# Kernel optimization log

Hardware: AMD Instinct MI355X
Metric: run time of the kernel (lower is better)

## Reference

```python
import jax, jax.numpy as jnp
import numpy as np

D_MODEL = 2048
N_HEADS = 32
N_KV_GROUPS = 8
D_HEAD = D_MODEL // N_HEADS  # 64
HEADS_PER_GROUP = N_HEADS // N_KV_GROUPS  # 4
BATCH, SEQ = 2, 2048


def setup_inputs() -> dict:
    key = jax.random.key(0)
    ks = jax.random.split(key, 5)
    s = 0.02
    return {
        "x": jax.random.normal(ks[0], (BATCH, SEQ, D_MODEL), jnp.float32),
        "W_q": jax.random.normal(ks[1], (N_HEADS * D_HEAD, D_MODEL), jnp.float32) * s,
        "W_k": jax.random.normal(ks[2], (N_KV_GROUPS * D_HEAD, D_MODEL), jnp.float32) * s,
        "W_v": jax.random.normal(ks[3], (N_KV_GROUPS * D_HEAD, D_MODEL), jnp.float32) * s,
        "W_o": jax.random.normal(ks[4], (D_MODEL, D_MODEL), jnp.float32) * s,
    }


def reference(x, W_q, W_k, W_v, W_o):
    B, S, _ = x.shape
    # Projections (nn.Linear: y = x @ W.T)
    Q = (x @ W_q.T).reshape(B, S, N_HEADS, D_HEAD)          # (B,S,H,D)
    K = (x @ W_k.T).reshape(B, S, N_KV_GROUPS, D_HEAD)       # (B,S,G,D)
    V = (x @ W_v.T).reshape(B, S, N_KV_GROUPS, D_HEAD)
    # Group Q heads: (B, G, Hg, S, D) so each KV group serves Hg query heads
    Qg = Q.transpose(0, 2, 1, 3).reshape(B, N_KV_GROUPS, HEADS_PER_GROUP, S, D_HEAD)
    Kg = K.transpose(0, 2, 1, 3)  # (B,G,S,D)
    Vg = V.transpose(0, 2, 1, 3)
    scale = 1.0 / np.sqrt(D_HEAD).astype(np.float32)
    # scores: (B,G,Hg,S,S) == expanded-KV scores without replicating K/V
    scores = jnp.einsum('bghqd,bgkd->bghqk', Qg, Kg) * scale
    weights = jax.nn.softmax(scores, axis=-1)
    context = jnp.einsum('bghqk,bgkd->bghqd', weights, Vg)   # (B,G,Hg,S,D)
    # back to (B,S,d_model)
    context = context.reshape(B, N_HEADS, S, D_HEAD).transpose(0, 2, 1, 3).reshape(B, S, D_MODEL)
    return context @ W_o.T
```

## Files before the change

kernel.cpp:

```cpp
#include <hip/hip_runtime.h>
#include <hip/hip_bf16.h>
#include <stdint.h>
#include <stddef.h>

typedef __hip_bfloat16 bf16;
typedef short bf16x8 __attribute__((ext_vector_type(8)));
typedef float f32x4 __attribute__((ext_vector_type(4)));

#define BB 2
#define SS 2048
#define DM 2048
#define NH 32
#define NG 8
#define DH 64
#define ROWS (BB * SS)
#define NQK 2560

#define ALPHA_QK 0.4246609001440095f

__device__ __forceinline__ void gload_lds16(const void* g, void* l) {
  __builtin_amdgcn_global_load_lds((const __attribute__((address_space(1))) void*)g,
                                   (__attribute__((address_space(3))) void*)l, 16, 0, 0);
}

__device__ __forceinline__ unsigned cvt_pk_bf16(float lo, float hi) {
  unsigned r;
  asm("v_cvt_pk_bf16_f32 %0, %1, %2" : "=v"(r) : "v"(lo), "v"(hi));
  return r;
}

__global__ __launch_bounds__(256) void cvt_all(const float* __restrict__ x,
                                               const float* __restrict__ wq,
                                               const float* __restrict__ wk,
                                               const float* __restrict__ wv,
                                               const float* __restrict__ wo,
                                               bf16* __restrict__ xb,
                                               bf16* __restrict__ wqkb,
                                               bf16* __restrict__ wvb,
                                               bf16* __restrict__ wob) {
  const int i = blockIdx.x * 256 + threadIdx.x;
  const float* src;
  bf16* dst;
  if (i < 2097152)       { src = x  + (size_t)i * 4;              dst = xb   + (size_t)i * 4; }
  else if (i < 3145728)  { size_t j = i - 2097152; src = wq + j * 4; dst = wqkb + j * 4; }
  else if (i < 3407872)  { size_t j = i - 3145728; src = wk + j * 4; dst = wqkb + 4194304 + j * 4; }
  else if (i < 3670016)  { size_t j = i - 3407872; src = wv + j * 4; dst = wvb  + j * 4; }
  else                   { size_t j = i - 3670016; src = wo + j * 4; dst = wob  + j * 4; }
  float4 v = *reinterpret_cast<const float4*>(src);
  bf16 t0 = __float2bfloat16(v.x), t1 = __float2bfloat16(v.y);
  bf16 t2 = __float2bfloat16(v.z), t3 = __float2bfloat16(v.w);
  ushort4 o;
  o.x = *reinterpret_cast<unsigned short*>(&t0);
  o.y = *reinterpret_cast<unsigned short*>(&t1);
  o.z = *reinterpret_cast<unsigned short*>(&t2);
  o.w = *reinterpret_cast<unsigned short*>(&t3);
  *reinterpret_cast<ushort4*>(dst) = o;
}

__device__ __forceinline__ void store_elem(float* C, size_t i, float v) { C[i] = v; }
__device__ __forceinline__ void store_elem(bf16* C, size_t i, float v) { C[i] = __float2bfloat16(v); }

template <typename CT>
__global__ __launch_bounds__(256) void gemm_bt(const bf16* __restrict__ A,
                                               const bf16* __restrict__ Bm,
                                               CT* __restrict__ C,
                                               int M, int N, int K, float alpha) {
  const int t = threadIdx.x;
  const int w = t >> 6, lane = t & 63, lg = lane >> 4, lr = lane & 15;
  const int wr = w >> 1, wc = w & 1;
  const int nwg = gridDim.x * gridDim.y;
  const int flat = blockIdx.y * gridDim.x + blockIdx.x;
  const int swz = (flat & 7) * (nwg >> 3) + (flat >> 3);
  const int rowA = (swz / gridDim.x) * 128, rowB = (swz % gridDim.x) * 128;
  __shared__ __align__(16) bf16 sA[3][128 * 32];
  __shared__ __align__(16) bf16 sB[3][128 * 32];
  f32x4 acc[4][4] = {};

  auto STAGE = [&](int bi, int k0) {
#pragma unroll
    for (int i = 0; i < 2; ++i) {
      const int c = i * 256 + t;
      const int r = c >> 2, slot = c & 3;
      const int ck = slot ^ ((r >> 1) & 3);
      gload_lds16(A + (size_t)(rowA + r) * K + k0 + ck * 8, &sA[bi][c * 8]);
      gload_lds16(Bm + (size_t)(rowB + r) * K + k0 + ck * 8, &sB[bi][c * 8]);
    }
  };

  const int nt = K / 32;
  STAGE(0, 0);
  STAGE(1, 32);
  STAGE(2, 64);

  for (int i = 0; i < nt; ++i) {
    if (i <= nt - 3)      asm volatile("s_waitcnt vmcnt(8)" ::: "memory");
    else if (i == nt - 2) asm volatile("s_waitcnt vmcnt(4)" ::: "memory");
    else                  asm volatile("s_waitcnt vmcnt(0)" ::: "memory");
    __builtin_amdgcn_s_barrier();

    const int bi = i % 3;
    bf16x8 af[4], bfv[4];
#pragma unroll
    for (int mi = 0; mi < 4; ++mi) {
      const int r = wr * 64 + mi * 16 + lr;
      af[mi] = *(const bf16x8*)&sA[bi][r * 32 + (lg ^ ((r >> 1) & 3)) * 8];
    }
#pragma unroll
    for (int ni = 0; ni < 4; ++ni) {
      const int r = wc * 64 + ni * 16 + lr;
      bfv[ni] = *(const bf16x8*)&sB[bi][r * 32 + (lg ^ ((r >> 1) & 3)) * 8];
    }
    asm volatile("s_waitcnt lgkmcnt(0)" ::: "memory");
    __builtin_amdgcn_sched_barrier(0);
    __builtin_amdgcn_s_barrier();
    if (i + 3 < nt) STAGE(bi, (i + 3) * 32);
#pragma unroll
    for (int mi = 0; mi < 4; ++mi)
#pragma unroll
      for (int ni = 0; ni < 4; ++ni)
        acc[mi][ni] = __builtin_amdgcn_mfma_f32_16x16x32_bf16(af[mi], bfv[ni], acc[mi][ni], 0, 0, 0);
  }

#pragma unroll
  for (int mi = 0; mi < 4; ++mi)
#pragma unroll
    for (int ni = 0; ni < 4; ++ni) {
      const int row0 = rowA + wr * 64 + mi * 16 + 4 * lg;
      const int col = rowB + wc * 64 + ni * 16 + lr;
#pragma unroll
      for (int r = 0; r < 4; ++r)
        store_elem(C, (size_t)(row0 + r) * N + col, acc[mi][ni][r] * alpha);
    }
}

__global__ __launch_bounds__(256, 3) void gqa_attn(const bf16* __restrict__ qk,
                                                   const bf16* __restrict__ vt,
                                                   bf16* __restrict__ ctx) {
  const int t = threadIdx.x, w = t >> 6, lane = t & 63, lg = lane >> 4, lr = lane & 15;
  const int flat = blockIdx.x;
  const int wg = (flat & 7) * 128 + (flat >> 3);
  const int head = wg >> 4;
  const int qb = (wg & 15) * 128;
  const int b = head >> 5, h = head & 31, g = h >> 2;
  const size_t LD = NQK;
  const bf16* Qp = qk + (size_t)b * SS * LD + h * 64;
  const bf16* Kp = qk + (size_t)b * SS * LD + 2048 + g * 64;
  const bf16* Vt = vt + (size_t)(g * 64) * ROWS + b * SS;

  __shared__ __align__(16) bf16 sK[2][64 * 64];
  __shared__ __align__(16) bf16 sV[2][64 * 64];
  __shared__ __align__(16) bf16 sP[4][32 * 72];

  bf16x8 qf[2][2];
#pragma unroll
  for (int mi = 0; mi < 2; ++mi) {
    const bf16* qrow = Qp + (size_t)(qb + w * 32 + mi * 16 + lr) * LD;
    qf[mi][0] = *(const bf16x8*)(qrow + lg * 8);
    qf[mi][1] = *(const bf16x8*)(qrow + 32 + lg * 8);
  }
  asm volatile("s_waitcnt vmcnt(0)" ::: "memory");

  float m_run[2], l_part[2];
  f32x4 o[2][4];
#pragma unroll
  for (int mi = 0; mi < 2; ++mi) {
    m_run[mi] = -3.0e38f;
    l_part[mi] = 0.0f;
#pragma unroll
    for (int dg = 0; dg < 4; ++dg) o[mi][dg] = (f32x4){0.f, 0.f, 0.f, 0.f};
  }

  auto STAGE = [&](int bi, int kt) {
#pragma unroll
    for (int i = 0; i < 2; ++i) {
      const int c = i * 256 + t;
      const int r = c >> 3, slot = c & 7;
      const int ck = slot ^ (r & 7);
      gload_lds16(Kp + (size_t)(kt * 64 + r) * LD + ck * 8, &sK[bi][c * 8]);
      gload_lds16(Vt + (size_t)r * ROWS + kt * 64 + ck * 8, &sV[bi][c * 8]);
    }
  };

  const int NT = SS / 64;
  STAGE(0, 0);
  int cur = 0;

  for (int kt = 0; kt < NT; ++kt) {
    if (kt + 1 < NT) {
      STAGE(cur ^ 1, kt + 1);
      asm volatile("s_waitcnt vmcnt(4)" ::: "memory");
    } else {
      asm volatile("s_waitcnt vmcnt(0)" ::: "memory");
    }
    __builtin_amdgcn_s_barrier();

    f32x4 s[2][4];
    __builtin_amdgcn_s_setprio(1);
#pragma unroll
    for (int cg = 0; cg < 4; ++cg) {
      const int kr = cg * 16 + lr;
      bf16x8 kf0 = *(const bf16x8*)&sK[cur][kr * 64 + ((lg) ^ (kr & 7)) * 8];
      bf16x8 kf1 = *(const bf16x8*)&sK[cur][kr * 64 + ((lg + 4) ^ (kr & 7)) * 8];
#pragma unroll
      for (int mi = 0; mi < 2; ++mi) {
        f32x4 z = {0.f, 0.f, 0.f, 0.f};
        z = __builtin_amdgcn_mfma_f32_16x16x32_bf16(kf0, qf[mi][0], z, 0, 0, 0);
        z = __builtin_amdgcn_mfma_f32_16x16x32_bf16(kf1, qf[mi][1], z, 0, 0, 0);
        s[mi][cg] = z;
      }
    }
    __builtin_amdgcn_s_setprio(0);

    float pm[2];
    bool ok = true;
#pragma unroll
    for (int mi = 0; mi < 2; ++mi) {
      float m0 = fmaxf(fmaxf(s[mi][0][0], s[mi][0][1]), fmaxf(s[mi][0][2], s[mi][0][3]));
      float m1 = fmaxf(fmaxf(s[mi][1][0], s[mi][1][1]), fmaxf(s[mi][1][2], s[mi][1][3]));
      float m2 = fmaxf(fmaxf(s[mi][2][0], s[mi][2][1]), fmaxf(s[mi][2][2], s[mi][2][3]));
      float m3 = fmaxf(fmaxf(s[mi][3][0], s[mi][3][1]), fmaxf(s[mi][3][2], s[mi][3][3]));
      pm[mi] = fmaxf(fmaxf(m0, m1), fmaxf(m2, m3));
      ok = ok && (pm[mi] <= m_run[mi] + 8.f);
    }
    if (!__all(ok)) {
#pragma unroll
      for (int mi = 0; mi < 2; ++mi) {
        float m = pm[mi];
        m = fmaxf(m, __shfl_xor(m, 16));
        m = fmaxf(m, __shfl_xor(m, 32));
        const float mn = fmaxf(m_run[mi], m);
        const float corr = __builtin_amdgcn_exp2f(m_run[mi] - mn);
        m_run[mi] = mn;
        l_part[mi] *= corr;
#pragma unroll
        for (int r = 0; r < 4; ++r) {
          const float co = __shfl(corr, 20 * lg + r);
#pragma unroll
          for (int dg = 0; dg < 4; ++dg) o[mi][dg][r] *= co;
        }
      }
    }

    bf16* sPw = sP[w];
#pragma unroll
    for (int mi = 0; mi < 2; ++mi) {
#pragma unroll
      for (int cg = 0; cg < 4; ++cg) {
        float p0 = __builtin_amdgcn_exp2f(s[mi][cg][0] - m_run[mi]);
        float p1 = __builtin_amdgcn_exp2f(s[mi][cg][1] - m_run[mi]);
        float p2 = __builtin_amdgcn_exp2f(s[mi][cg][2] - m_run[mi]);
        float p3 = __builtin_amdgcn_exp2f(s[mi][cg][3] - m_run[mi]);
        l_part[mi] += (p0 + p1) + (p2 + p3);
        uint2 pk;
        pk.x = cvt_pk_bf16(p0, p1);
        pk.y = cvt_pk_bf16(p2, p3);
        *(uint2*)&sPw[(mi * 16 + lr) * 72 + cg * 16 + 4 * lg] = pk;
      }
    }

#pragma unroll
    for (int kc = 0; kc < 2; ++kc) {
      bf16x8 pf[2];
#pragma unroll
      for (int mi = 0; mi < 2; ++mi)
        pf[mi] = *(const bf16x8*)&sPw[(mi * 16 + lr) * 72 + kc * 32 + lg * 8];
      __builtin_amdgcn_s_setprio(1);
#pragma unroll
      for (int dg = 0; dg < 4; ++dg) {
        const int vr = dg * 16 + lr;
        bf16x8 vf = *(const bf16x8*)&sV[cur][vr * 64 + ((kc * 4 + lg) ^ (vr & 7)) * 8];
#pragma unroll
        for (int mi = 0; mi < 2; ++mi)
          o[mi][dg] = __builtin_amdgcn_mfma_f32_16x16x32_bf16(pf[mi], vf, o[mi][dg], 0, 0, 0);
      }
      __builtin_amdgcn_s_setprio(0);
    }

    asm volatile("s_waitcnt lgkmcnt(0)" ::: "memory");
    __builtin_amdgcn_sched_barrier(0);
    __builtin_amdgcn_s_barrier();
    cur ^= 1;
  }

#pragma unroll
  for (int mi = 0; mi < 2; ++mi) {
    float l = l_part[mi];
    l += __shfl_xor(l, 16);
    l += __shfl_xor(l, 32);
    const int orow0 = b * SS + qb + w * 32 + mi * 16 + 4 * lg;
#pragma unroll
    for (int r = 0; r < 4; ++r) {
      const float lo = __shfl(l, 20 * lg + r);
      const float inv = 1.0f / lo;
      const int row = orow0 + r;
#pragma unroll
      for (int dg = 0; dg < 4; ++dg) {
        const int col = h * 64 + dg * 16 + lr;
        ctx[(size_t)row * DM + col] = __float2bfloat16(o[mi][dg][r] * inv);
      }
    }
  }
}

extern "C" void kernel_launch(void* const* d_in, const int* in_sizes, int n_in,
                              void* d_out, int out_size, void* d_ws, size_t ws_size,
                              hipStream_t stream) {
  const float* x   = (const float*)d_in[0];
  const float* W_q = (const float*)d_in[1];
  const float* W_k = (const float*)d_in[2];
  const float* W_v = (const float*)d_in[3];
  const float* W_o = (const float*)d_in[4];
  float* out = (float*)d_out;

  char* ws = (char*)d_ws;
  bf16* xb    = (bf16*)ws; ws += (size_t)ROWS * DM * 2;
  bf16* wqk   = (bf16*)ws; ws += (size_t)NQK * DM * 2;
  bf16* wv    = (bf16*)ws; ws += (size_t)(NG * DH) * DM * 2;
  bf16* wo    = (bf16*)ws; ws += (size_t)DM * DM * 2;
  bf16* qkbuf = (bf16*)ws; ws += (size_t)ROWS * NQK * 2;
  bf16* vtb   = (bf16*)ws; ws += (size_t)(NG * DH) * ROWS * 2;
  bf16* ctx   = (bf16*)ws; ws += (size_t)ROWS * DM * 2;

  cvt_all<<<18432, 256, 0, stream>>>(x, W_q, W_k, W_v, W_o, xb, wqk, wv, wo);

  gemm_bt<bf16><<<dim3(NQK / 128, ROWS / 128), 256, 0, stream>>>(xb, wqk, qkbuf, ROWS, NQK, DM, ALPHA_QK);
  gemm_bt<bf16><<<dim3(ROWS / 128, (NG * DH) / 128), 256, 0, stream>>>(wv, xb, vtb, NG * DH, ROWS, DM, 1.0f);
  gqa_attn<<<1024, 256, 0, stream>>>(qkbuf, vtb, ctx);
  gemm_bt<float><<<dim3(DM / 128, ROWS / 128), 256, 0, stream>>>(ctx, wo, out, ROWS, DM, DM, 1.0f);
}
```

Before: 244.3 us.

## Fuse QK and V projection GEMMs into one launch; use max3 in softmax

Merges the QK projection GEMM (640 tiles) and the transposed V projection GEMM (128 tiles) into a single 768-block kernel. Each block picks its sub-problem from a swizzled index, which removes one launch and lets the small V GEMM fill idle CUs beside the larger one instead of running as a low-occupancy tail. The GEMM body becomes a shared device function with hardcoded tile grids. It also replaces the fmaxf tree in the attention row-max with v_max3_f32 inline asm to cut VALU instructions.

```diff
diff --git a/kernel.cpp b/kernel.cpp
--- a/kernel.cpp
+++ b/kernel.cpp
@@ -26,6 +26,12 @@
 __device__ __forceinline__ unsigned cvt_pk_bf16(float lo, float hi) {
   unsigned r;
   asm("v_cvt_pk_bf16_f32 %0, %1, %2" : "=v"(r) : "v"(lo), "v"(hi));
+  return r;
+}
+
+__device__ __forceinline__ float max3f(float a, float b, float c) {
+  float r;
+  asm("v_max3_f32 %0, %1, %2, %3" : "=v"(r) : "v"(a), "v"(b), "v"(c));
   return r;
 }
 
@@ -61,19 +67,14 @@
 __device__ __forceinline__ void store_elem(bf16* C, size_t i, float v) { C[i] = __float2bfloat16(v); }
 
 template <typename CT>
-__global__ __launch_bounds__(256) void gemm_bt(const bf16* __restrict__ A,
-                                               const bf16* __restrict__ Bm,
-                                               CT* __restrict__ C,
-                                               int M, int N, int K, float alpha) {
+__device__ __forceinline__ void gemm_body(const bf16* __restrict__ A,
+                                          const bf16* __restrict__ Bm,
+                                          CT* __restrict__ C,
+                                          int rowA, int rowB, int N, int K, float alpha,
+                                          bf16 (*sA)[128 * 32], bf16 (*sB)[128 * 32]) {
   const int t = threadIdx.x;
   const int w = t >> 6, lane = t & 63, lg = lane >> 4, lr = lane & 15;
   const int wr = w >> 1, wc = w & 1;
-  const int nwg = gridDim.x * gridDim.y;
-  const int flat = blockIdx.y * gridDim.x + blockIdx.x;
-  const int swz = (flat & 7) * (nwg >> 3) + (flat >> 3);
-  const int rowA = (swz / gridDim.x) * 128, rowB = (swz % gridDim.x) * 128;
-  __shared__ __align__(16) bf16 sA[3][128 * 32];
-  __shared__ __align__(16) bf16 sB[3][128 * 32];
   f32x4 acc[4][4] = {};
 
   auto STAGE = [&](int bi, int k0) {
@@ -131,6 +132,37 @@
       for (int r = 0; r < 4; ++r)
         store_elem(C, (size_t)(row0 + r) * N + col, acc[mi][ni][r] * alpha);
     }
+}
+
+__global__ __launch_bounds__(256) void gemm_qkv(const bf16* __restrict__ xb,
+                                                const bf16* __restrict__ wqk,
+                                                const bf16* __restrict__ wv,
+                                                bf16* __restrict__ qkbuf,
+                                                bf16* __restrict__ vtb) {
+  __shared__ __align__(16) bf16 sA[3][128 * 32];
+  __shared__ __align__(16) bf16 sB[3][128 * 32];
+  const int flat = blockIdx.x;
+  const int swz = (flat & 7) * 96 + (flat >> 3);
+  if (swz < 640) {
+    const int rowA = (swz / 20) * 128, rowB = (swz % 20) * 128;
+    gemm_body<bf16>(xb, wqk, qkbuf, rowA, rowB, NQK, DM, ALPHA_QK, sA, sB);
+  } else {
+    const int j = swz - 640;
+    const int rowA = (j / 32) * 128, rowB = (j % 32) * 128;
+    gemm_body<bf16>(wv, xb, vtb, rowA, rowB, ROWS, DM, 1.0f, sA, sB);
+  }
+}
+
+__global__ __launch_bounds__(256) void gemm_out(const bf16* __restrict__ ctx,
+                                                const bf16* __restrict__ wo,
+                                                float* __restrict__ out) {
+  __shared__ __align__(16) bf16 sA[3][128 * 32];
+  __shared__ __align__(16) bf16 sB[3][128 * 32];
+  const int nwg = gridDim.x;
+  const int flat = blockIdx.x;
+  const int swz = (flat & 7) * (nwg >> 3) + (flat >> 3);
+  const int rowA = (swz / 16) * 128, rowB = (swz % 16) * 128;
+  gemm_body<float>(ctx, wo, out, rowA, rowB, DM, DM, 1.0f, sA, sB);
 }
 
 __global__ __launch_bounds__(256, 3) void gqa_attn(const bf16* __restrict__ qk,
@@ -215,11 +247,12 @@
     bool ok = true;
 #pragma unroll
     for (int mi = 0; mi < 2; ++mi) {
-      float m0 = fmaxf(fmaxf(s[mi][0][0], s[mi][0][1]), fmaxf(s[mi][0][2], s[mi][0][3]));
-      float m1 = fmaxf(fmaxf(s[mi][1][0], s[mi][1][1]), fmaxf(s[mi][1][2], s[mi][1][3]));
-      float m2 = fmaxf(fmaxf(s[mi][2][0], s[mi][2][1]), fmaxf(s[mi][2][2], s[mi][2][3]));
-      float m3 = fmaxf(fmaxf(s[mi][3][0], s[mi][3][1]), fmaxf(s[mi][3][2], s[mi][3][3]));
-      pm[mi] = fmaxf(fmaxf(m0, m1), fmaxf(m2, m3));
+      float a0 = max3f(s[mi][0][0], s[mi][0][1], s[mi][0][2]);
+      float a1 = max3f(s[mi][0][3], s[mi][1][0], s[mi][1][1]);
+      float a2 = max3f(s[mi][1][2], s[mi][1][3], s[mi][2][0]);
+      float a3 = max3f(s[mi][2][1], s[mi][2][2], s[mi][2][3]);
+      float a4 = max3f(s[mi][3][0], s[mi][3][1], s[mi][3][2]);
+      pm[mi] = fmaxf(max3f(a0, a1, a2), max3f(a3, a4, s[mi][3][3]));
       ok = ok && (pm[mi] <= m_run[mi] + 8.f);
     }
     if (!__all(ok)) {
@@ -323,8 +356,7 @@
 
   cvt_all<<<18432, 256, 0, stream>>>(x, W_q, W_k, W_v, W_o, xb, wqk, wv, wo);
 
-  gemm_bt<bf16><<<dim3(NQK / 128, ROWS / 128), 256, 0, stream>>>(xb, wqk, qkbuf, ROWS, NQK, DM, ALPHA_QK);
-  gemm_bt<bf16><<<dim3(ROWS / 128, (NG * DH) / 128), 256, 0, stream>>>(wv, xb, vtb, NG * DH, ROWS, DM, 1.0f);
+  gemm_qkv<<<768, 256, 0, stream>>>(xb, wqk, wv, qkbuf, vtb);
   gqa_attn<<<1024, 256, 0, stream>>>(qkbuf, vtb, ctx);
-  gemm_bt<float><<<dim3(DM / 128, ROWS / 128), 256, 0, stream>>>(ctx, wo, out, ROWS, DM, DM, 1.0f);
-}
+  gemm_out<<<512, 256, 0, stream>>>(ctx, wo, out);
+}
```

Measured after the change: 220.3 us. 9.9% less time.
